# Optimization experiments

Hardware: AMD Instinct MI355X
Metric: run time of the kernel (lower is better)

## Reference

```python
import jax, jax.numpy as jnp
import numpy as np

D = 64   # hidden dim (input_dim == hidden_dims[i] == 64)
L = 6    # GNN layers per NBFNet
EPS = 1e-5

def _layer_norm(x, g, b):
    m = jnp.mean(x, axis=-1, keepdims=True)
    v = jnp.var(x, axis=-1, keepdims=True)
    return (x - m) * jax.lax.rsqrt(v + EPS) * g + b

def _conv(x, boundary, relation, edge_index, edge_type, W, b, g, bt):
    # GeneralizedRelationalConv: distmult message, sum aggregation with
    # boundary self-loop message, linear([input, agg]) -> LayerNorm -> ReLU.
    src, dst = edge_index[0], edge_index[1]
    msg = x[:, src, :] * relation[:, edge_type, :]                # [B,E,D]
    agg = boundary + jnp.zeros_like(x).at[:, dst, :].add(msg)     # edge_weight == 1
    out = jnp.einsum('bnf,fo->bno', jnp.concatenate([x, agg], axis=-1), W) + b
    return jax.nn.relu(_layer_norm(out, g, bt))

def _rel_model(q_rel, rel_edge_index, rel_edge_type, num_rel_nodes,
               rel_emb, Wr, br, gr, btr):
    # RelNBFNet.bellmanford: query = ones, boundary scatter at query relation node.
    B = q_rel.shape[0]
    query = jnp.ones((B, D), dtype=rel_emb.dtype)
    boundary = jnp.zeros((B, num_rel_nodes, D), rel_emb.dtype).at[jnp.arange(B), q_rel].add(query)
    relation = jnp.broadcast_to(rel_emb[None], (B,) + rel_emb.shape)  # dependent=False embedding
    def step(x, p):
        W, b, g, bt = p
        h = _conv(x, boundary, relation, rel_edge_index, rel_edge_type, W, b, g, bt)
        return h + x, None  # short_cut residual
    x, _ = jax.lax.scan(step, boundary, (Wr, br, gr, btr))
    return x  # [B, R, D]  (concat_hidden=False -> hiddens[-1])

def _ent_model(rel_repr, h_index, r_index, t_index, edge_index, edge_type,
               num_nodes, Wp1, bp1, Wp2, bp2, We, be, ge, bte, W1, b1, W2, b2):
    B = h_index.shape[0]
    query = rel_repr[jnp.arange(B), r_index]                      # [B,D]
    boundary = jnp.zeros((B, num_nodes, D), query.dtype).at[jnp.arange(B), h_index].add(query)
    def step(x, p):
        wp1, b1p, wp2, b2p, W, b, g, bt = p
        # project_relations=True: per-layer 2-layer MLP on relation representations
        rel = jax.nn.relu(rel_repr @ wp1 + b1p) @ wp2 + b2p       # [B,R,D]
        h = _conv(x, boundary, rel, edge_index, edge_type, W, b, g, bt)
        return h + x, None
    x, _ = jax.lax.scan(step, boundary, (Wp1, bp1, Wp2, bp2, We, be, ge, bte))
    node_query = jnp.broadcast_to(query[:, None, :], x.shape)
    feat = jnp.concatenate([x, node_query], axis=-1)              # [B,N,2D]
    feat = feat[jnp.arange(B)[:, None], t_index]                  # gather tails [B,K,2D]
    h = jax.nn.relu(feat @ W1 + b1)                               # num_mlp_layers=2
    return (h @ W2 + b2)[..., 0]                                  # [B,K]

def setup_inputs() -> dict:
    key = jax.random.key(0)
    ks = jax.random.split(key, 16)
    B, K, N, E, R, Er = 4, 256, 20000, 200000, 200, 4000
    ND = 100  # direct relations; R = 2*ND
    h = jax.random.randint(ks[0], (B,), 0, N)
    r = jax.random.randint(ks[1], (B,), 0, ND)
    t = jax.random.randint(ks[2], (B, K), 0, N)
    batch = jnp.stack([jnp.broadcast_to(h[:, None], (B, K)), t,
                       jnp.broadcast_to(r[:, None], (B, K))], axis=-1)
    s = 0.05
    return dict(
        batch=batch,
        edge_index=jax.random.randint(ks[3], (2, E), 0, N),
        edge_type=jax.random.randint(ks[4], (E,), 0, R),
        rel_edge_index=jax.random.randint(ks[5], (2, Er), 0, R),
        rel_edge_type=jax.random.randint(ks[6], (Er,), 0, 4),
        num_nodes=N, num_rel_nodes=R,
        rel_emb=jax.random.normal(ks[7], (4, D)) * s,
        Wr=jax.random.normal(ks[8], (L, 2 * D, D)) * s,
        br=jnp.zeros((L, D)), gr=jnp.ones((L, D)), btr=jnp.zeros((L, D)),
        Wp1=jax.random.normal(ks[9], (L, D, D)) * s,
        bp1=jnp.zeros((L, D)),
        Wp2=jax.random.normal(ks[10], (L, D, D)) * s,
        bp2=jnp.zeros((L, D)),
        We=jax.random.normal(ks[11], (L, 2 * D, D)) * s,
        be=jnp.zeros((L, D)), ge=jnp.ones((L, D)), bte=jnp.zeros((L, D)),
        W1=jax.random.normal(ks[12], (2 * D, 2 * D)) * s,
        b1=jnp.zeros((2 * D,)),
        W2=jax.random.normal(ks[13], (2 * D, 1)) * s,
        b2=jnp.zeros((1,)),
    )

def reference(batch, edge_index, edge_type, rel_edge_index, rel_edge_type,
              num_nodes, num_rel_nodes,
              rel_emb, Wr, br, gr, btr,
              Wp1, bp1, Wp2, bp2, We, be, ge, bte, W1, b1, W2, b2):
    # batch holds tail-negative triples (h, t, r) with constant h and r per row,
    # so negative_sample_to_tail is the identity here (eval mode: no edge removal).
    h_index = batch[:, 0, 0]
    t_index = batch[:, :, 1]
    r_index = batch[:, 0, 2]
    rel_repr = _rel_model(r_index, rel_edge_index, rel_edge_type, num_rel_nodes,
                          rel_emb, Wr, br, gr, btr)
    return _ent_model(rel_repr, h_index, r_index, t_index, edge_index, edge_type,
                      num_nodes, Wp1, bp1, Wp2, bp2, We, be, ge, bte, W1, b1, W2, b2)
```

## Files before the change

kernel.cpp:

```cpp
#include <hip/hip_runtime.h>
#include <hip/hip_bf16.h>

#define D_   64
#define L_   6
#define B_   4
#define K_   256
#define NN   20000
#define EE   200000
#define RR   200
#define ER_  4000
#define EPS_ 1e-5f

typedef unsigned short u16;
typedef unsigned int   u32;
typedef short bf16x8 __attribute__((ext_vector_type(8)));
typedef float f32x4  __attribute__((ext_vector_type(4)));

__device__ __forceinline__ u16 f2bf(float f) {
    u32 u = __float_as_uint(f);
    u += 0x7FFF + ((u >> 16) & 1);
    return (u16)(u >> 16);
}
__device__ __forceinline__ u32 pack2bf(float a, float b) {
    return (u32)f2bf(a) | ((u32)f2bf(b) << 16);
}
__device__ __forceinline__ float bflo(u32 u) { return __uint_as_float(u << 16); }
__device__ __forceinline__ float bfhi(u32 u) { return __uint_as_float(u & 0xFFFF0000u); }

__global__ __launch_bounds__(256)
void k_zero2(int* __restrict__ ec, int* __restrict__ rc) {
    int i = blockIdx.x * 256 + threadIdx.x;
    if (i < NN) ec[i] = 0;
    else if (i < NN + RR) rc[i - NN] = 0;
}

__global__ __launch_bounds__(256)
void k_hist2(const int* __restrict__ ei, const int* __restrict__ rei,
             int* __restrict__ ec, int* __restrict__ rc) {
    int g = blockIdx.x * 256 + threadIdx.x;
    if (g < EE) atomicAdd(&ec[ei[EE + g]], 1);
    else if (g < EE + ER_) atomicAdd(&rc[rei[ER_ + (g - EE)]], 1);
}

__global__ __launch_bounds__(256)
void k_scan1_2(const int* __restrict__ e_counts, int* __restrict__ e_pre, int* __restrict__ e_bs,
               const int* __restrict__ r_counts, int* __restrict__ r_pre, int* __restrict__ r_bs,
               int ent_nb) {
    __shared__ int tsum[256];
    const int* counts; int* pre; int* bs; int n; int blk;
    if ((int)blockIdx.x < ent_nb) { counts = e_counts; pre = e_pre; bs = e_bs; n = NN; blk = blockIdx.x; }
    else                          { counts = r_counts; pre = r_pre; bs = r_bs; n = RR; blk = 0; }
    int tid = threadIdx.x;
    int base = blk * 1024 + tid * 4;
    int c0 = 0, c1 = 0, c2 = 0, c3 = 0;
    if (base + 0 < n) c0 = counts[base + 0];
    if (base + 1 < n) c1 = counts[base + 1];
    if (base + 2 < n) c2 = counts[base + 2];
    if (base + 3 < n) c3 = counts[base + 3];
    tsum[tid] = c0 + c1 + c2 + c3;
    __syncthreads();
    if (tid == 0) {
        int acc = 0;
        for (int i = 0; i < 256; i++) { int t = tsum[i]; tsum[i] = acc; acc += t; }
    }
    __syncthreads();
    int run = tsum[tid];
    if (base + 0 < n) pre[base + 0] = run; run += c0;
    if (base + 1 < n) pre[base + 1] = run; run += c1;
    if (base + 2 < n) pre[base + 2] = run; run += c2;
    if (base + 3 < n) pre[base + 3] = run; run += c3;
    if (tid == 255) bs[blk] = run;
}

__global__ __launch_bounds__(64)
void k_scan2_2(int* __restrict__ eb, int enb, int* __restrict__ etot,
               int* __restrict__ rb, int rnb, int* __restrict__ rtot) {
    if (threadIdx.x == 0) {
        int acc = 0;
        for (int i = 0; i < enb; i++) { int t = eb[i]; eb[i] = acc; acc += t; }
        *etot = acc;
    }
    if (threadIdx.x == 1) {
        int acc = 0;
        for (int i = 0; i < rnb; i++) { int t = rb[i]; rb[i] = acc; acc += t; }
        *rtot = acc;
    }
}

__global__ __launch_bounds__(256)
void k_scan3_2(int* __restrict__ e_rp, const int* __restrict__ e_bs, int* __restrict__ e_cur,
               int* __restrict__ r_rp, const int* __restrict__ r_bs, int* __restrict__ r_cur) {
    int i = blockIdx.x * 256 + threadIdx.x;
    if (i < NN) {
        int v = e_rp[i] + e_bs[i >> 10];
        e_rp[i] = v; e_cur[i] = v;
    } else if (i < NN + RR) {
        int j = i - NN;
        int v = r_rp[j] + r_bs[j >> 10];
        r_rp[j] = v; r_cur[j] = v;
    }
}

__global__ __launch_bounds__(256)
void k_fill2(const int* __restrict__ ei, const int* __restrict__ et,
             const int* __restrict__ rei, const int* __restrict__ ret,
             int* __restrict__ e_cur, int* __restrict__ r_cur,
             int* __restrict__ e_packed, int* __restrict__ r_packed) {
    int g = blockIdx.x * 256 + threadIdx.x;
    if (g < EE) {
        int pos = atomicAdd(&e_cur[ei[EE + g]], 1);
        e_packed[pos] = ei[g] | (et[g] << 15);
    } else if (g < EE + ER_) {
        int h = g - EE;
        int pos = atomicAdd(&r_cur[rei[ER_ + h]], 1);
        r_packed[pos] = rei[h] | (ret[h] << 15);
    }
}

template<int NNODES, int MODE, bool FIRST>
__global__ __launch_bounds__(512)
void k_layer6(const float* __restrict__ xin, float* __restrict__ xout,
              const u16* __restrict__ xbin, u16* __restrict__ xbout,
              const void* __restrict__ relv,
              const int* __restrict__ rowptr, const int* __restrict__ packed,
              const float* __restrict__ query, const int* __restrict__ batch,
              const float* __restrict__ W, const float* __restrict__ bias,
              const float* __restrict__ gw, const float* __restrict__ bt) {
    __shared__ u16 Wt[2][64][72];
    __shared__ u16 As[32][72];
    __shared__ u16 Xs[32][72];
    __shared__ float LNbuf[32][68];
    const int tid   = threadIdx.x;
    const int node0 = blockIdx.x * 8;
    const int lane  = tid & 63;
    const int wv    = tid >> 6;

    int bn0 = batch[0 * K_ * 3 + (MODE ? 0 : 2)];
    int bn1 = batch[1 * K_ * 3 + (MODE ? 0 : 2)];
    int bn2 = batch[2 * K_ * 3 + (MODE ? 0 : 2)];
    int bn3 = batch[3 * K_ * 3 + (MODE ? 0 : 2)];

    {
        int n = lane;
        int half = wv >> 2, k16 = (wv & 3) * 16;
        u32 buf[8];
        #pragma unroll
        for (int j2 = 0; j2 < 8; j2++) {
            float w0 = W[(half * 64 + k16 + 2 * j2    ) * 64 + n];
            float w1 = W[(half * 64 + k16 + 2 * j2 + 1) * 64 + n];
            buf[j2] = pack2bf(w0, w1);
        }
        uint4* dst = reinterpret_cast<uint4*>(&Wt[half][n][k16]);
        dst[0] = make_uint4(buf[0], buf[1], buf[2], buf[3]);
        dst[1] = make_uint4(buf[4], buf[5], buf[6], buf[7]);
    }

    for (int u = tid; u < 256; u += 512) {
        int m = u >> 3, o8 = (u & 7) * 8;
        int b = m >> 3, node = node0 + (m & 7);
        uint4 v = make_uint4(0, 0, 0, 0);
        if (node < NNODES) {
            if constexpr (FIRST) {
                int bnb = (b==0)?bn0:(b==1)?bn1:(b==2)?bn2:bn3;
                if (node == bnb) {
                    if constexpr (MODE == 1) {
                        const float* q = query + b * 64 + o8;
                        v = make_uint4(pack2bf(q[0], q[1]), pack2bf(q[2], q[3]),
                                       pack2bf(q[4], q[5]), pack2bf(q[6], q[7]));
                    } else {
                        v = make_uint4(0x3F803F80u, 0x3F803F80u, 0x3F803F80u, 0x3F803F80u);
                    }
                }
            } else if constexpr (MODE == 1) {
                v = *reinterpret_cast<const uint4*>(
                    xbin + ((size_t)b * NNODES + node) * 64 + o8);
            } else {
                const float* src = xin + ((size_t)b * NNODES + node) * 64 + o8;
                float4 x0 = *reinterpret_cast<const float4*>(src);
                float4 x1 = *reinterpret_cast<const float4*>(src + 4);
                v = make_uint4(pack2bf(x0.x, x0.y), pack2bf(x0.z, x0.w),
                               pack2bf(x1.x, x1.y), pack2bf(x1.z, x1.w));
            }
        }
        *reinterpret_cast<uint4*>(&Xs[m][o8]) = v;
    }

    const int slot = lane >> 3;
    const int d8   = lane & 7;

    float qreg[4][8];
    if constexpr (MODE == 1) {
        #pragma unroll
        for (int b = 0; b < 4; b++) {
            float4 q0 = *reinterpret_cast<const float4*>(query + b * 64 + d8 * 8);
            float4 q1 = *reinterpret_cast<const float4*>(query + b * 64 + d8 * 8 + 4);
            qreg[b][0]=q0.x; qreg[b][1]=q0.y; qreg[b][2]=q0.z; qreg[b][3]=q0.w;
            qreg[b][4]=q1.x; qreg[b][5]=q1.y; qreg[b][6]=q1.z; qreg[b][7]=q1.w;
        }
    }

    {
        int node = node0 + wv;
        float acc[4][8];
        #pragma unroll
        for (int b = 0; b < 4; b++)
            #pragma unroll
            for (int i = 0; i < 8; i++) acc[b][i] = 0.f;

        if (node < NNODES) {
            int beg = rowptr[node], end = rowptr[node + 1];
            for (int e0 = beg; e0 < end; e0 += 16) {
                #pragma unroll
                for (int half = 0; half < 2; half++) {
                    int e = e0 + half * 8 + slot;
                    if (e < end) {
                        int p = packed[e];
                        int src = p & 0x7FFF;
                        int et  = p >> 15;
                        if constexpr (MODE == 1) {
                            const u16* rb = (const u16*)relv;
                            if constexpr (FIRST) {
                                #pragma unroll
                                for (int b = 0; b < 4; b++) {
                                    int bnb = (b==0)?bn0:(b==1)?bn1:(b==2)?bn2:bn3;
                                    if (src == bnb) {
                                        uint4 rv = *reinterpret_cast<const uint4*>(
                                            rb + ((size_t)(b * RR + et)) * 64 + d8 * 8);
                                        acc[b][0] = fmaf(qreg[b][0], bflo(rv.x), acc[b][0]);
                                        acc[b][1] = fmaf(qreg[b][1], bfhi(rv.x), acc[b][1]);
                                        acc[b][2] = fmaf(qreg[b][2], bflo(rv.y), acc[b][2]);
                                        acc[b][3] = fmaf(qreg[b][3], bfhi(rv.y), acc[b][3]);
                                        acc[b][4] = fmaf(qreg[b][4], bflo(rv.z), acc[b][4]);
                                        acc[b][5] = fmaf(qreg[b][5], bfhi(rv.z), acc[b][5]);
                                        acc[b][6] = fmaf(qreg[b][6], bflo(rv.w), acc[b][6]);
                                        acc[b][7] = fmaf(qreg[b][7], bfhi(rv.w), acc[b][7]);
                                    }
                                }
                            } else {
                                #pragma unroll
                                for (int b = 0; b < 4; b++) {
                                    uint4 xv = *reinterpret_cast<const uint4*>(
                                        xbin + ((size_t)(b * NNODES + src)) * 64 + d8 * 8);
                                    uint4 rv = *reinterpret_cast<const uint4*>(
                                        ((const u16*)relv) + ((size_t)(b * RR + et)) * 64 + d8 * 8);
                                    acc[b][0] = fmaf(bflo(xv.x), bflo(rv.x), acc[b][0]);
                                    acc[b][1] = fmaf(bfhi(xv.x), bfhi(rv.x), acc[b][1]);
                                    acc[b][2] = fmaf(bflo(xv.y), bflo(rv.y), acc[b][2]);
                                    acc[b][3] = fmaf(bfhi(xv.y), bfhi(rv.y), acc[b][3]);
                                    acc[b][4] = fmaf(bflo(xv.z), bflo(rv.z), acc[b][4]);
                                    acc[b][5] = fmaf(bfhi(xv.z), bfhi(rv.z), acc[b][5]);
                                    acc[b][6] = fmaf(bflo(xv.w), bflo(rv.w), acc[b][6]);
                                    acc[b][7] = fmaf(bfhi(xv.w), bfhi(rv.w), acc[b][7]);
                                }
                            }
                        } else {
                            const float* re = (const float*)relv;
                            if constexpr (FIRST) {
                                bool m0 = (src == bn0), m1 = (src == bn1),
                                     m2 = (src == bn2), m3 = (src == bn3);
                                if (m0 | m1 | m2 | m3) {
                                    float4 r0 = *reinterpret_cast<const float4*>(re + et * 64 + d8 * 8);
                                    float4 r1 = *reinterpret_cast<const float4*>(re + et * 64 + d8 * 8 + 4);
                                    float rr[8] = {r0.x,r0.y,r0.z,r0.w,r1.x,r1.y,r1.z,r1.w};
                                    if (m0) {
                                        #pragma unroll
                                        for (int i = 0; i < 8; i++) acc[0][i] += rr[i];
                                    }
                                    if (m1) {
                                        #pragma unroll
                                        for (int i = 0; i < 8; i++) acc[1][i] += rr[i];
                                    }
                                    if (m2) {
                                        #pragma unroll
                                        for (int i = 0; i < 8; i++) acc[2][i] += rr[i];
                                    }
                                    if (m3) {
                                        #pragma unroll
                                        for (int i = 0; i < 8; i++) acc[3][i] += rr[i];
                                    }
                                }
                            } else {
                                float4 r0 = *reinterpret_cast<const float4*>(re + et * 64 + d8 * 8);
                                float4 r1 = *reinterpret_cast<const float4*>(re + et * 64 + d8 * 8 + 4);
                                #pragma unroll
                                for (int b = 0; b < 4; b++) {
                                    const float* xr = xin + ((size_t)(b * NNODES + src)) * 64 + d8 * 8;
                                    float4 x0 = *reinterpret_cast<const float4*>(xr);
                                    float4 x1 = *reinterpret_cast<const float4*>(xr + 4);
                                    acc[b][0] = fmaf(x0.x, r0.x, acc[b][0]);
                                    acc[b][1] = fmaf(x0.y, r0.y, acc[b][1]);
                                    acc[b][2] = fmaf(x0.z, r0.z, acc[b][2]);
                                    acc[b][3] = fmaf(x0.w, r0.w, acc[b][3]);
                                    acc[b][4] = fmaf(x1.x, r1.x, acc[b][4]);
                                    acc[b][5] = fmaf(x1.y, r1.y, acc[b][5]);
                                    acc[b][6] = fmaf(x1.z, r1.z, acc[b][6]);
                                    acc[b][7] = fmaf(x1.w, r1.w, acc[b][7]);
                                }
                            }
                        }
                    }
                }
            }
        }

        #pragma unroll
        for (int b = 0; b < 4; b++)
            #pragma unroll
            for (int i = 0; i < 8; i++) {
                float v = acc[b][i];
                v += __shfl_xor(v, 8);
                v += __shfl_xor(v, 16);
                v += __shfl_xor(v, 32);
                acc[b][i] = v;
            }

        if (slot < 4) {
            float out[8];
            #pragma unroll
            for (int i = 0; i < 8; i++)
                out[i] = (slot==0) ? acc[0][i] : (slot==1) ? acc[1][i]
                       : (slot==2) ? acc[2][i] : acc[3][i];
            int bnb = (slot==0)?bn0:(slot==1)?bn1:(slot==2)?bn2:bn3;
            if (node < NNODES && node == bnb) {
                if constexpr (MODE == 1) {
                    #pragma unroll
                    for (int i = 0; i < 8; i++)
                        out[i] += (slot==0)?qreg[0][i]:(slot==1)?qreg[1][i]
                                 :(slot==2)?qreg[2][i]:qreg[3][i];
                } else {
                    #pragma unroll
                    for (int i = 0; i < 8; i++) out[i] += 1.0f;
                }
            }
            int m = slot * 8 + wv;
            *reinterpret_cast<uint4*>(&As[m][d8 * 8]) =
                make_uint4(pack2bf(out[0], out[1]), pack2bf(out[2], out[3]),
                           pack2bf(out[4], out[5]), pack2bf(out[6], out[7]));
        }
    }
    __syncthreads();

    const int al = lane & 15;
    const int ag = lane >> 4;
    const int mt = wv >> 2;
    const int nt = wv & 3;
    f32x4 acc4 = (f32x4){0.f, 0.f, 0.f, 0.f};
    {
        bf16x8 a0 = *reinterpret_cast<const bf16x8*>(&As[mt * 16 + al][ag * 8]);
        bf16x8 a1 = *reinterpret_cast<const bf16x8*>(&As[mt * 16 + al][32 + ag * 8]);
        bf16x8 b0 = *reinterpret_cast<const bf16x8*>(&Wt[1][nt * 16 + al][ag * 8]);
        bf16x8 b1 = *reinterpret_cast<const bf16x8*>(&Wt[1][nt * 16 + al][32 + ag * 8]);
        acc4 = __builtin_amdgcn_mfma_f32_16x16x32_bf16(a0, b0, acc4, 0, 0, 0);
        acc4 = __builtin_amdgcn_mfma_f32_16x16x32_bf16(a1, b1, acc4, 0, 0, 0);
        bf16x8 c0 = *reinterpret_cast<const bf16x8*>(&Xs[mt * 16 + al][ag * 8]);
        bf16x8 c1 = *reinterpret_cast<const bf16x8*>(&Xs[mt * 16 + al][32 + ag * 8]);
        bf16x8 d0 = *reinterpret_cast<const bf16x8*>(&Wt[0][nt * 16 + al][ag * 8]);
        bf16x8 d1 = *reinterpret_cast<const bf16x8*>(&Wt[0][nt * 16 + al][32 + ag * 8]);
        acc4 = __builtin_amdgcn_mfma_f32_16x16x32_bf16(c0, d0, acc4, 0, 0, 0);
        acc4 = __builtin_amdgcn_mfma_f32_16x16x32_bf16(c1, d1, acc4, 0, 0, 0);
    }
    #pragma unroll
    for (int reg = 0; reg < 4; reg++)
        LNbuf[mt * 16 + ag * 4 + reg][nt * 16 + al] = acc4[reg];
    __syncthreads();

    {
        int row = wv * 4 + (lane >> 4);
        int tx  = lane & 15;
        int b = row >> 3, node = node0 + (row & 7);
        float o[4];
        float s1 = 0.f, s2 = 0.f;
        #pragma unroll
        for (int i = 0; i < 4; i++) {
            o[i] = LNbuf[row][tx * 4 + i] + bias[tx * 4 + i];
            s1 += o[i];
            s2 += o[i] * o[i];
        }
        s1 += __shfl_xor(s1, 1); s2 += __shfl_xor(s2, 1);
        s1 += __shfl_xor(s1, 2); s2 += __shfl_xor(s2, 2);
        s1 += __shfl_xor(s1, 4); s2 += __shfl_xor(s2, 4);
        s1 += __shfl_xor(s1, 8); s2 += __shfl_xor(s2, 8);
        float mean = s1 * (1.f / 64.f);
        float var  = s2 * (1.f / 64.f) - mean * mean;
        float inv  = rsqrtf(var + EPS_);
        if (node < NNODES) {
            int bnb = (b==0)?bn0:(b==1)?bn1:(b==2)?bn2:bn3;
            size_t ro = ((size_t)b * NNODES + node) * 64;
            float r[4];
            if constexpr (FIRST) {
                #pragma unroll
                for (int i = 0; i < 4; i++) r[i] = 0.f;
                if (node == bnb) {
                    if constexpr (MODE == 1) {
                        float4 q = *reinterpret_cast<const float4*>(query + b * 64 + tx * 4);
                        r[0] = q.x; r[1] = q.y; r[2] = q.z; r[3] = q.w;
                    } else {
                        r[0] = r[1] = r[2] = r[3] = 1.0f;
                    }
                }
            } else {
                float4 xv = *reinterpret_cast<const float4*>(xin + ro + tx * 4);
                r[0] = xv.x; r[1] = xv.y; r[2] = xv.z; r[3] = xv.w;
            }
            float nv[4];
            #pragma unroll
            for (int i = 0; i < 4; i++) {
                float h = (o[i] - mean) * inv * gw[tx * 4 + i] + bt[tx * 4 + i];
                h = fmaxf(h, 0.f);
                nv[i] = r[i] + h;
            }
            *reinterpret_cast<float4*>(&xout[ro + tx * 4]) =
                make_float4(nv[0], nv[1], nv[2], nv[3]);
            if constexpr (MODE == 1) {
                ushort4 b4;
                b4.x = f2bf(nv[0]); b4.y = f2bf(nv[1]);
                b4.z = f2bf(nv[2]); b4.w = f2bf(nv[3]);
                *reinterpret_cast<ushort4*>(&xbout[ro + tx * 4]) = b4;
            }
        }
    }
}

__global__ __launch_bounds__(64)
void k_rel_mlp_all(const float* __restrict__ rel_repr,
                   const float* __restrict__ Wp1, const float* __restrict__ bp1,
                   const float* __restrict__ Wp2, const float* __restrict__ bp2,
                   u16* __restrict__ out) {
    __shared__ float rowv[64];
    __shared__ float hid[64];
    int l     = blockIdx.x / (B_ * RR);
    int rowid = blockIdx.x % (B_ * RR);
    int d = threadIdx.x;
    const float* w1 = Wp1 + l * 4096;
    const float* w2 = Wp2 + l * 4096;
    rowv[d] = rel_repr[rowid * 64 + d];
    __syncthreads();
    float acc = bp1[l * 64 + d];
    for (int k = 0; k < 64; k++) acc = fmaf(rowv[k], w1[k * 64 + d], acc);
    hid[d] = fmaxf(acc, 0.f);
    __syncthreads();
    float o = bp2[l * 64 + d];
    for (int k = 0; k < 64; k++) o = fmaf(hid[k], w2[k * 64 + d], o);
    out[(size_t)l * B_ * RR * 64 + rowid * 64 + d] = f2bf(o);
}

__global__ __launch_bounds__(256)
void k_query(const float* __restrict__ rel_repr, const int* __restrict__ batch,
             float* __restrict__ query) {
    int tid = threadIdx.x;
    int b = tid >> 6;
    int d = tid & 63;
    int r = batch[b * K_ * 3 + 2];
    query[b * 64 + d] = rel_repr[(b * RR + r) * 64 + d];
}

__global__ __launch_bounds__(128)
void k_final(const float* __restrict__ x, const float* __restrict__ query,
             const int* __restrict__ batch,
             const float* __restrict__ W1, const float* __restrict__ b1,
             const float* __restrict__ W2, const float* __restrict__ b2,
             float* __restrict__ out) {
    __shared__ float feat[128];
    __shared__ float partial[2];
    int pair = blockIdx.x;
    int b = pair / K_;
    int t = batch[pair * 3 + 1];
    int d = threadIdx.x;
    feat[d] = (d < 64) ? x[(size_t)(b * NN + t) * 64 + d] : query[b * 64 + (d - 64)];
    __syncthreads();
    float h = b1[d];
    for (int i = 0; i < 128; i++) h = fmaf(feat[i], W1[i * 128 + d], h);
    h = fmaxf(h, 0.f);
    float v = h * W2[d];
    #pragma unroll
    for (int off = 1; off < 64; off <<= 1) v += __shfl_xor(v, off);
    if ((d & 63) == 0) partial[d >> 6] = v;
    __syncthreads();
    if (d == 0) out[pair] = partial[0] + partial[1] + b2[0];
}

extern "C" void kernel_launch(void* const* d_in, const int* in_sizes, int n_in,
                              void* d_out, int out_size, void* d_ws, size_t ws_size,
                              hipStream_t stream) {
    const int* batch      = (const int*)d_in[0];
    const int* edge_index = (const int*)d_in[1];
    const int* edge_type  = (const int*)d_in[2];
    const int* rel_ei     = (const int*)d_in[3];
    const int* rel_et     = (const int*)d_in[4];
    const float* rel_emb = (const float*)d_in[7];
    const float* Wr  = (const float*)d_in[8];
    const float* br  = (const float*)d_in[9];
    const float* gr  = (const float*)d_in[10];
    const float* btr = (const float*)d_in[11];
    const float* Wp1 = (const float*)d_in[12];
    const float* bp1 = (const float*)d_in[13];
    const float* Wp2 = (const float*)d_in[14];
    const float* bp2 = (const float*)d_in[15];
    const float* We  = (const float*)d_in[16];
    const float* be  = (const float*)d_in[17];
    const float* ge  = (const float*)d_in[18];
    const float* bte = (const float*)d_in[19];
    const float* W1  = (const float*)d_in[20];
    const float* b1  = (const float*)d_in[21];
    const float* W2  = (const float*)d_in[22];
    const float* b2  = (const float*)d_in[23];

    float* ws = (float*)d_ws;
    float* rel_buf0 = ws;
    float* rel_buf1 = rel_buf0 + 51200;
    float* query    = rel_buf1 + 51200;
    float* x0       = query + 256;
    float* x1       = x0 + (size_t)B_ * NN * 64;
    u16*   xb0      = (u16*)(x1 + (size_t)B_ * NN * 64);
    u16*   xb1      = xb0 + (size_t)B_ * NN * 64;
    u16*   rel_all  = xb1 + (size_t)B_ * NN * 64;
    int*   iw       = (int*)(rel_all + (size_t)L_ * B_ * RR * 64);

    int* ent_counts  = iw;
    int* ent_rowptr  = ent_counts + NN;
    int* ent_bsums   = ent_rowptr + NN + 1;
    int* ent_packed  = ent_bsums + 32;
    int* rel_counts  = ent_packed + EE;
    int* rel_rowptr  = rel_counts + RR;
    int* rel_bsums   = rel_rowptr + RR + 1;
    int* rel_packed  = rel_bsums + 8;

    const int ENT_NB = (NN + 1023) / 1024;
    const int REL_NB = (RR + 1023) / 1024;

    k_zero2<<<(NN + RR + 255) / 256, 256, 0, stream>>>(ent_counts, rel_counts);
    k_hist2<<<(EE + ER_ + 255) / 256, 256, 0, stream>>>(edge_index, rel_ei, ent_counts, rel_counts);
    k_scan1_2<<<ENT_NB + REL_NB, 256, 0, stream>>>(ent_counts, ent_rowptr, ent_bsums,
                                                   rel_counts, rel_rowptr, rel_bsums, ENT_NB);
    k_scan2_2<<<1, 64, 0, stream>>>(ent_bsums, ENT_NB, ent_rowptr + NN,
                                    rel_bsums, REL_NB, rel_rowptr + RR);
    k_scan3_2<<<(NN + RR + 255) / 256, 256, 0, stream>>>(ent_rowptr, ent_bsums, ent_counts,
                                                         rel_rowptr, rel_bsums, rel_counts);
    k_fill2<<<(EE + ER_ + 255) / 256, 256, 0, stream>>>(edge_index, edge_type, rel_ei, rel_et,
                                                        ent_counts, rel_counts, ent_packed, rel_packed);

    float* rf[2] = {rel_buf0, rel_buf1};
    const int RGRID = (RR + 7) / 8;
    k_layer6<RR, 0, true><<<RGRID, 512, 0, stream>>>(
        nullptr, rf[0], nullptr, nullptr, rel_emb,
        rel_rowptr, rel_packed, nullptr, batch,
        Wr, br, gr, btr);
    int rc = 0;
    for (int l = 1; l < L_; ++l) {
        k_layer6<RR, 0, false><<<RGRID, 512, 0, stream>>>(
            rf[rc], rf[rc ^ 1], nullptr, nullptr, rel_emb,
            rel_rowptr, rel_packed, nullptr, batch,
            Wr + l * 8192, br + l * 64, gr + l * 64, btr + l * 64);
        rc ^= 1;
    }
    float* rel_final = rf[rc];

    k_query<<<1, 256, 0, stream>>>(rel_final, batch, query);
    k_rel_mlp_all<<<L_ * B_ * RR, 64, 0, stream>>>(rel_final, Wp1, bp1, Wp2, bp2, rel_all);
    float* xf[2] = {x0, x1};
    u16*   xh[2] = {xb0, xb1};
    const int EGRID = (NN + 7) / 8;
    k_layer6<NN, 1, true><<<EGRID, 512, 0, stream>>>(
        nullptr, xf[0], nullptr, xh[0], rel_all,
        ent_rowptr, ent_packed, query, batch,
        We, be, ge, bte);
    int ec = 0;
    for (int l = 1; l < L_; ++l) {
        k_layer6<NN, 1, false><<<EGRID, 512, 0, stream>>>(
            xf[ec], xf[ec ^ 1], xh[ec], xh[ec ^ 1],
            rel_all + (size_t)l * B_ * RR * 64,
            ent_rowptr, ent_packed, query, batch,
            We + l * 8192, be + l * 64, ge + l * 64, bte + l * 64);
        ec ^= 1;
    }
    k_final<<<B_ * K_, 128, 0, stream>>>(xf[ec], query, batch, W1, b1, W2, b2,
                                         (float*)d_out);
}
```

Baseline: 420.5 us.

## Shrink layer blocks to 4 nodes with a reused weight buffer and early loads

```diff
diff --git a/kernel.cpp b/kernel.cpp
--- a/kernel.cpp
+++ b/kernel.cpp
@@ -118,20 +118,20 @@
 }
 
 template<int NNODES, int MODE, bool FIRST>
-__global__ __launch_bounds__(512)
-void k_layer6(const float* __restrict__ xin, float* __restrict__ xout,
+__global__ __launch_bounds__(256)
+void k_layer9(const float* __restrict__ xin, float* __restrict__ xout,
               const u16* __restrict__ xbin, u16* __restrict__ xbout,
               const void* __restrict__ relv,
               const int* __restrict__ rowptr, const int* __restrict__ packed,
               const float* __restrict__ query, const int* __restrict__ batch,
               const float* __restrict__ W, const float* __restrict__ bias,
               const float* __restrict__ gw, const float* __restrict__ bt) {
-    __shared__ u16 Wt[2][64][72];
-    __shared__ u16 As[32][72];
-    __shared__ u16 Xs[32][72];
-    __shared__ float LNbuf[32][68];
+    __shared__ u16 Wt[64][72];
+    __shared__ u16 As[16][72];
+    __shared__ u16 Xs[16][72];
+    __shared__ float LNbuf[16][68];
     const int tid   = threadIdx.x;
-    const int node0 = blockIdx.x * 8;
+    const int node0 = blockIdx.x * 4;
     const int lane  = tid & 63;
     const int wv    = tid >> 6;
 
@@ -140,24 +140,37 @@
     int bn2 = batch[2 * K_ * 3 + (MODE ? 0 : 2)];
     int bn3 = batch[3 * K_ * 3 + (MODE ? 0 : 2)];
 
+    const int gnode = node0 + wv;
+    int beg = 0, end = 0;
+    if (gnode < NNODES) { beg = rowptr[gnode]; end = rowptr[gnode + 1]; }
+
+    const int erow  = wv * 4 + (lane >> 4);
+    const int tx    = lane & 15;
+    float4 resf = make_float4(0.f, 0.f, 0.f, 0.f);
+    if constexpr (!FIRST) {
+        int b = erow >> 2, nd = node0 + (erow & 3);
+        if (nd < NNODES)
+            resf = *reinterpret_cast<const float4*>(
+                xin + ((size_t)b * NNODES + nd) * 64 + tx * 4);
+    }
+
     {
-        int n = lane;
-        int half = wv >> 2, k16 = (wv & 3) * 16;
+        int n = lane, k16 = wv * 16;
         u32 buf[8];
         #pragma unroll
         for (int j2 = 0; j2 < 8; j2++) {
-            float w0 = W[(half * 64 + k16 + 2 * j2    ) * 64 + n];
-            float w1 = W[(half * 64 + k16 + 2 * j2 + 1) * 64 + n];
+            float w0 = W[(64 + k16 + 2 * j2    ) * 64 + n];
+            float w1 = W[(64 + k16 + 2 * j2 + 1) * 64 + n];
             buf[j2] = pack2bf(w0, w1);
         }
-        uint4* dst = reinterpret_cast<uint4*>(&Wt[half][n][k16]);
+        uint4* dst = reinterpret_cast<uint4*>(&Wt[n][k16]);
         dst[0] = make_uint4(buf[0], buf[1], buf[2], buf[3]);
         dst[1] = make_uint4(buf[4], buf[5], buf[6], buf[7]);
     }
 
-    for (int u = tid; u < 256; u += 512) {
-        int m = u >> 3, o8 = (u & 7) * 8;
-        int b = m >> 3, node = node0 + (m & 7);
+    if (tid < 128) {
+        int m = tid >> 3, o8 = (tid & 7) * 8;
+        int b = m >> 2, node = node0 + (m & 3);
         uint4 v = make_uint4(0, 0, 0, 0);
         if (node < NNODES) {
             if constexpr (FIRST) {
@@ -200,102 +213,98 @@
     }
 
     {
-        int node = node0 + wv;
         float acc[4][8];
         #pragma unroll
         for (int b = 0; b < 4; b++)
             #pragma unroll
             for (int i = 0; i < 8; i++) acc[b][i] = 0.f;
 
-        if (node < NNODES) {
-            int beg = rowptr[node], end = rowptr[node + 1];
-            for (int e0 = beg; e0 < end; e0 += 16) {
-                #pragma unroll
-                for (int half = 0; half < 2; half++) {
-                    int e = e0 + half * 8 + slot;
-                    if (e < end) {
-                        int p = packed[e];
-                        int src = p & 0x7FFF;
-                        int et  = p >> 15;
-                        if constexpr (MODE == 1) {
-                            const u16* rb = (const u16*)relv;
-                            if constexpr (FIRST) {
-                                #pragma unroll
-                                for (int b = 0; b < 4; b++) {
-                                    int bnb = (b==0)?bn0:(b==1)?bn1:(b==2)?bn2:bn3;
-                                    if (src == bnb) {
-                                        uint4 rv = *reinterpret_cast<const uint4*>(
-                                            rb + ((size_t)(b * RR + et)) * 64 + d8 * 8);
-                                        acc[b][0] = fmaf(qreg[b][0], bflo(rv.x), acc[b][0]);
-                                        acc[b][1] = fmaf(qreg[b][1], bfhi(rv.x), acc[b][1]);
-                                        acc[b][2] = fmaf(qreg[b][2], bflo(rv.y), acc[b][2]);
-                                        acc[b][3] = fmaf(qreg[b][3], bfhi(rv.y), acc[b][3]);
-                                        acc[b][4] = fmaf(qreg[b][4], bflo(rv.z), acc[b][4]);
-                                        acc[b][5] = fmaf(qreg[b][5], bfhi(rv.z), acc[b][5]);
-                                        acc[b][6] = fmaf(qreg[b][6], bflo(rv.w), acc[b][6]);
-                                        acc[b][7] = fmaf(qreg[b][7], bfhi(rv.w), acc[b][7]);
-                                    }
-                                }
-                            } else {
-                                #pragma unroll
-                                for (int b = 0; b < 4; b++) {
-                                    uint4 xv = *reinterpret_cast<const uint4*>(
-                                        xbin + ((size_t)(b * NNODES + src)) * 64 + d8 * 8);
+        for (int e0 = beg; e0 < end; e0 += 16) {
+            #pragma unroll
+            for (int half = 0; half < 2; half++) {
+                int e = e0 + half * 8 + slot;
+                if (e < end) {
+                    int p = packed[e];
+                    int src = p & 0x7FFF;
+                    int et  = p >> 15;
+                    if constexpr (MODE == 1) {
+                        const u16* rb = (const u16*)relv;
+                        if constexpr (FIRST) {
+                            #pragma unroll
+                            for (int b = 0; b < 4; b++) {
+                                int bnb = (b==0)?bn0:(b==1)?bn1:(b==2)?bn2:bn3;
+                                if (src == bnb) {
                                     uint4 rv = *reinterpret_cast<const uint4*>(
-                                        ((const u16*)relv) + ((size_t)(b * RR + et)) * 64 + d8 * 8);
-                                    acc[b][0] = fmaf(bflo(xv.x), bflo(rv.x), acc[b][0]);
-                                    acc[b][1] = fmaf(bfhi(xv.x), bfhi(rv.x), acc[b][1]);
-                                    acc[b][2] = fmaf(bflo(xv.y), bflo(rv.y), acc[b][2]);
-                                    acc[b][3] = fmaf(bfhi(xv.y), bfhi(rv.y), acc[b][3]);
-                                    acc[b][4] = fmaf(bflo(xv.z), bflo(rv.z), acc[b][4]);
-                                    acc[b][5] = fmaf(bfhi(xv.z), bfhi(rv.z), acc[b][5]);
-                                    acc[b][6] = fmaf(bflo(xv.w), bflo(rv.w), acc[b][6]);
-                                    acc[b][7] = fmaf(bfhi(xv.w), bfhi(rv.w), acc[b][7]);
+                                        rb + ((size_t)(b * RR + et)) * 64 + d8 * 8);
+                                    acc[b][0] = fmaf(qreg[b][0], bflo(rv.x), acc[b][0]);
+                                    acc[b][1] = fmaf(qreg[b][1], bfhi(rv.x), acc[b][1]);
+                                    acc[b][2] = fmaf(qreg[b][2], bflo(rv.y), acc[b][2]);
+                                    acc[b][3] = fmaf(qreg[b][3], bfhi(rv.y), acc[b][3]);
+                                    acc[b][4] = fmaf(qreg[b][4], bflo(rv.z), acc[b][4]);
+                                    acc[b][5] = fmaf(qreg[b][5], bfhi(rv.z), acc[b][5]);
+                                    acc[b][6] = fmaf(qreg[b][6], bflo(rv.w), acc[b][6]);
+                                    acc[b][7] = fmaf(qreg[b][7], bfhi(rv.w), acc[b][7]);
                                 }
                             }
                         } else {
-                            const float* re = (const float*)relv;
-                            if constexpr (FIRST) {
-                                bool m0 = (src == bn0), m1 = (src == bn1),
-                                     m2 = (src == bn2), m3 = (src == bn3);
-                                if (m0 | m1 | m2 | m3) {
-                                    float4 r0 = *reinterpret_cast<const float4*>(re + et * 64 + d8 * 8);
-                                    float4 r1 = *reinterpret_cast<const float4*>(re + et * 64 + d8 * 8 + 4);
-                                    float rr[8] = {r0.x,r0.y,r0.z,r0.w,r1.x,r1.y,r1.z,r1.w};
-                                    if (m0) {
-                                        #pragma unroll
-                                        for (int i = 0; i < 8; i++) acc[0][i] += rr[i];
-                                    }
-                                    if (m1) {
-                                        #pragma unroll
-                                        for (int i = 0; i < 8; i++) acc[1][i] += rr[i];
-                                    }
-                                    if (m2) {
-                                        #pragma unroll
-                                        for (int i = 0; i < 8; i++) acc[2][i] += rr[i];
-                                    }
-                                    if (m3) {
-                                        #pragma unroll
-                                        for (int i = 0; i < 8; i++) acc[3][i] += rr[i];
-                                    }
-                                }
-                            } else {
+                            #pragma unroll
+                            for (int b = 0; b < 4; b++) {
+                                uint4 xv = *reinterpret_cast<const uint4*>(
+                                    xbin + ((size_t)(b * NNODES + src)) * 64 + d8 * 8);
+                                uint4 rv = *reinterpret_cast<const uint4*>(
+                                    ((const u16*)relv) + ((size_t)(b * RR + et)) * 64 + d8 * 8);
+                                acc[b][0] = fmaf(bflo(xv.x), bflo(rv.x), acc[b][0]);
+                                acc[b][1] = fmaf(bfhi(xv.x), bfhi(rv.x), acc[b][1]);
+                                acc[b][2] = fmaf(bflo(xv.y), bflo(rv.y), acc[b][2]);
+                                acc[b][3] = fmaf(bfhi(xv.y), bfhi(rv.y), acc[b][3]);
+                                acc[b][4] = fmaf(bflo(xv.z), bflo(rv.z), acc[b][4]);
+                                acc[b][5] = fmaf(bfhi(xv.z), bfhi(rv.z), acc[b][5]);
+                                acc[b][6] = fmaf(bflo(xv.w), bflo(rv.w), acc[b][6]);
+                                acc[b][7] = fmaf(bfhi(xv.w), bfhi(rv.w), acc[b][7]);
+                            }
+                        }
+                    } else {
+                        const float* re = (const float*)relv;
+                        if constexpr (FIRST) {
+                            bool m0 = (src == bn0), m1 = (src == bn1),
+                                 m2 = (src == bn2), m3 = (src == bn3);
+                            if (m0 | m1 | m2 | m3) {
                                 float4 r0 = *reinterpret_cast<const float4*>(re + et * 64 + d8 * 8);
                                 float4 r1 = *reinterpret_cast<const float4*>(re + et * 64 + d8 * 8 + 4);
-                                #pragma unroll
-                                for (int b = 0; b < 4; b++) {
-                                    const float* xr = xin + ((size_t)(b * NNODES + src)) * 64 + d8 * 8;
-                                    float4 x0 = *reinterpret_cast<const float4*>(xr);
-                                    float4 x1 = *reinterpret_cast<const float4*>(xr + 4);
-                                    acc[b][0] = fmaf(x0.x, r0.x, acc[b][0]);
-                                    acc[b][1] = fmaf(x0.y, r0.y, acc[b][1]);
-                                    acc[b][2] = fmaf(x0.z, r0.z, acc[b][2]);
-                                    acc[b][3] = fmaf(x0.w, r0.w, acc[b][3]);
-                                    acc[b][4] = fmaf(x1.x, r1.x, acc[b][4]);
-                                    acc[b][5] = fmaf(x1.y, r1.y, acc[b][5]);
-                                    acc[b][6] = fmaf(x1.z, r1.z, acc[b][6]);
-                                    acc[b][7] = fmaf(x1.w, r1.w, acc[b][7]);
+                                float rr[8] = {r0.x,r0.y,r0.z,r0.w,r1.x,r1.y,r1.z,r1.w};
+                                if (m0) {
+                                    #pragma unroll
+                                    for (int i = 0; i < 8; i++) acc[0][i] += rr[i];
                                 }
+                                if (m1) {
+                                    #pragma unroll
+                                    for (int i = 0; i < 8; i++) acc[1][i] += rr[i];
+                                }
+                                if (m2) {
+                                    #pragma unroll
+                                    for (int i = 0; i < 8; i++) acc[2][i] += rr[i];
+                                }
+                                if (m3) {
+                                    #pragma unroll
+                                    for (int i = 0; i < 8; i++) acc[3][i] += rr[i];
+                                }
+                            }
+                        } else {
+                            float4 r0 = *reinterpret_cast<const float4*>(re + et * 64 + d8 * 8);
+                            float4 r1 = *reinterpret_cast<const float4*>(re + et * 64 + d8 * 8 + 4);
+                            #pragma unroll
+                            for (int b = 0; b < 4; b++) {
+                                const float* xr = xin + ((size_t)(b * NNODES + src)) * 64 + d8 * 8;
+                                float4 x0 = *reinterpret_cast<const float4*>(xr);
+                                float4 x1 = *reinterpret_cast<const float4*>(xr + 4);
+                                acc[b][0] = fmaf(x0.x, r0.x, acc[b][0]);
+                                acc[b][1] = fmaf(x0.y, r0.y, acc[b][1]);
+                                acc[b][2] = fmaf(x0.z, r0.z, acc[b][2]);
+                                acc[b][3] = fmaf(x0.w, r0.w, acc[b][3]);
+                                acc[b][4] = fmaf(x1.x, r1.x, acc[b][4]);
+                                acc[b][5] = fmaf(x1.y, r1.y, acc[b][5]);
+                                acc[b][6] = fmaf(x1.z, r1.z, acc[b][6]);
+                                acc[b][7] = fmaf(x1.w, r1.w, acc[b][7]);
                             }
                         }
                     }
@@ -321,7 +330,7 @@
                 out[i] = (slot==0) ? acc[0][i] : (slot==1) ? acc[1][i]
                        : (slot==2) ? acc[2][i] : acc[3][i];
             int bnb = (slot==0)?bn0:(slot==1)?bn1:(slot==2)?bn2:bn3;
-            if (node < NNODES && node == bnb) {
+            if (gnode < NNODES && gnode == bnb) {
                 if constexpr (MODE == 1) {
                     #pragma unroll
                     for (int i = 0; i < 8; i++)
@@ -332,7 +341,7 @@
                     for (int i = 0; i < 8; i++) out[i] += 1.0f;
                 }
             }
-            int m = slot * 8 + wv;
+            int m = slot * 4 + wv;
             *reinterpret_cast<uint4*>(&As[m][d8 * 8]) =
                 make_uint4(pack2bf(out[0], out[1]), pack2bf(out[2], out[3]),
                            pack2bf(out[4], out[5]), pack2bf(out[6], out[7]));
@@ -342,32 +351,49 @@
 
     const int al = lane & 15;
     const int ag = lane >> 4;
-    const int mt = wv >> 2;
-    const int nt = wv & 3;
+    const int nt = wv;
     f32x4 acc4 = (f32x4){0.f, 0.f, 0.f, 0.f};
     {
-        bf16x8 a0 = *reinterpret_cast<const bf16x8*>(&As[mt * 16 + al][ag * 8]);
-        bf16x8 a1 = *reinterpret_cast<const bf16x8*>(&As[mt * 16 + al][32 + ag * 8]);
-        bf16x8 b0 = *reinterpret_cast<const bf16x8*>(&Wt[1][nt * 16 + al][ag * 8]);
-        bf16x8 b1 = *reinterpret_cast<const bf16x8*>(&Wt[1][nt * 16 + al][32 + ag * 8]);
+        bf16x8 a0 = *reinterpret_cast<const bf16x8*>(&As[al][ag * 8]);
+        bf16x8 a1 = *reinterpret_cast<const bf16x8*>(&As[al][32 + ag * 8]);
+        bf16x8 b0 = *reinterpret_cast<const bf16x8*>(&Wt[nt * 16 + al][ag * 8]);
+        bf16x8 b1 = *reinterpret_cast<const bf16x8*>(&Wt[nt * 16 + al][32 + ag * 8]);
         acc4 = __builtin_amdgcn_mfma_f32_16x16x32_bf16(a0, b0, acc4, 0, 0, 0);
         acc4 = __builtin_amdgcn_mfma_f32_16x16x32_bf16(a1, b1, acc4, 0, 0, 0);
-        bf16x8 c0 = *reinterpret_cast<const bf16x8*>(&Xs[mt * 16 + al][ag * 8]);
-        bf16x8 c1 = *reinterpret_cast<const bf16x8*>(&Xs[mt * 16 + al][32 + ag * 8]);
-        bf16x8 d0 = *reinterpret_cast<const bf16x8*>(&Wt[0][nt * 16 + al][ag * 8]);
-        bf16x8 d1 = *reinterpret_cast<const bf16x8*>(&Wt[0][nt * 16 + al][32 + ag * 8]);
-        acc4 = __builtin_amdgcn_mfma_f32_16x16x32_bf16(c0, d0, acc4, 0, 0, 0);
-        acc4 = __builtin_amdgcn_mfma_f32_16x16x32_bf16(c1, d1, acc4, 0, 0, 0);
+    }
+    __syncthreads();
+
+    {
+        int n = lane, k16 = wv * 16;
+        u32 buf[8];
+        #pragma unroll
+        for (int j2 = 0; j2 < 8; j2++) {
+            float w0 = W[(k16 + 2 * j2    ) * 64 + n];
+            float w1 = W[(k16 + 2 * j2 + 1) * 64 + n];
+            buf[j2] = pack2bf(w0, w1);
+        }
+        uint4* dst = reinterpret_cast<uint4*>(&Wt[n][k16]);
+        dst[0] = make_uint4(buf[0], buf[1], buf[2], buf[3]);
+        dst[1] = make_uint4(buf[4], buf[5], buf[6], buf[7]);
+    }
+    __syncthreads();
+
+    {
+        bf16x8 x0 = *reinterpret_cast<const bf16x8*>(&Xs[al][ag * 8]);
+        bf16x8 x1 = *reinterpret_cast<const bf16x8*>(&Xs[al][32 + ag * 8]);
+        bf16x8 b0 = *reinterpret_cast<const bf16x8*>(&Wt[nt * 16 + al][ag * 8]);
+        bf16x8 b1 = *reinterpret_cast<const bf16x8*>(&Wt[nt * 16 + al][32 + ag * 8]);
+        acc4 = __builtin_amdgcn_mfma_f32_16x16x32_bf16(x0, b0, acc4, 0, 0, 0);
+        acc4 = __builtin_amdgcn_mfma_f32_16x16x32_bf16(x1, b1, acc4, 0, 0, 0);
     }
     #pragma unroll
     for (int reg = 0; reg < 4; reg++)
-        LNbuf[mt * 16 + ag * 4 + reg][nt * 16 + al] = acc4[reg];
+        LNbuf[ag * 4 + reg][nt * 16 + al] = acc4[reg];
     __syncthreads();
 
     {
-        int row = wv * 4 + (lane >> 4);
-        int tx  = lane & 15;
-        int b = row >> 3, node = node0 + (row & 7);
+        int row = erow;
+        int b = row >> 2, node = node0 + (row & 3);
         float o[4];
         float s1 = 0.f, s2 = 0.f;
         #pragma unroll
@@ -386,10 +412,9 @@
         if (node < NNODES) {
             int bnb = (b==0)?bn0:(b==1)?bn1:(b==2)?bn2:bn3;
             size_t ro = ((size_t)b * NNODES + node) * 64;
-            float r[4];
+            float r[4] = {resf.x, resf.y, resf.z, resf.w};
             if constexpr (FIRST) {
-                #pragma unroll
-                for (int i = 0; i < 4; i++) r[i] = 0.f;
+                r[0] = r[1] = r[2] = r[3] = 0.f;
                 if (node == bnb) {
                     if constexpr (MODE == 1) {
                         float4 q = *reinterpret_cast<const float4*>(query + b * 64 + tx * 4);
@@ -398,9 +423,6 @@
                         r[0] = r[1] = r[2] = r[3] = 1.0f;
                     }
                 }
-            } else {
-                float4 xv = *reinterpret_cast<const float4*>(xin + ro + tx * 4);
-                r[0] = xv.x; r[1] = xv.y; r[2] = xv.z; r[3] = xv.w;
             }
             float nv[4];
             #pragma unroll
@@ -540,14 +562,14 @@
                                                         ent_counts, rel_counts, ent_packed, rel_packed);
 
     float* rf[2] = {rel_buf0, rel_buf1};
-    const int RGRID = (RR + 7) / 8;
-    k_layer6<RR, 0, true><<<RGRID, 512, 0, stream>>>(
+    const int RGRID = (RR + 3) / 4;
+    k_layer9<RR, 0, true><<<RGRID, 256, 0, stream>>>(
         nullptr, rf[0], nullptr, nullptr, rel_emb,
         rel_rowptr, rel_packed, nullptr, batch,
         Wr, br, gr, btr);
     int rc = 0;
     for (int l = 1; l < L_; ++l) {
-        k_layer6<RR, 0, false><<<RGRID, 512, 0, stream>>>(
+        k_layer9<RR, 0, false><<<RGRID, 256, 0, stream>>>(
             rf[rc], rf[rc ^ 1], nullptr, nullptr, rel_emb,
             rel_rowptr, rel_packed, nullptr, batch,
             Wr + l * 8192, br + l * 64, gr + l * 64, btr + l * 64);
@@ -559,14 +581,14 @@
     k_rel_mlp_all<<<L_ * B_ * RR, 64, 0, stream>>>(rel_final, Wp1, bp1, Wp2, bp2, rel_all);
     float* xf[2] = {x0, x1};
     u16*   xh[2] = {xb0, xb1};
-    const int EGRID = (NN + 7) / 8;
-    k_layer6<NN, 1, true><<<EGRID, 512, 0, stream>>>(
+    const int EGRID = (NN + 3) / 4;
+    k_layer9<NN, 1, true><<<EGRID, 256, 0, stream>>>(
         nullptr, xf[0], nullptr, xh[0], rel_all,
         ent_rowptr, ent_packed, query, batch,
         We, be, ge, bte);
     int ec = 0;
     for (int l = 1; l < L_; ++l) {
-        k_layer6<NN, 1, false><<<EGRID, 512, 0, stream>>>(
+        k_layer9<NN, 1, false><<<EGRID, 256, 0, stream>>>(
             xf[ec], xf[ec ^ 1], xh[ec], xh[ec ^ 1],
             rel_all + (size_t)l * B_ * RR * 64,
             ent_rowptr, ent_packed, query, batch,
```

After: 400.7 us (median of 2 runs). 4.7% less time.
